# Kernel tuning notes

Hardware: AMD Instinct MI355X
Metric: run time of the kernel (lower is better)

## Reference

```python
import jax, jax.numpy as jnp
import numpy as np

D_MODEL, D_STATE, D_CONV, EXPAND = 1024, 16, 4, 2
D_INNER = EXPAND * D_MODEL
B, L = 2, 2048


def setup_inputs() -> dict:
    key = jax.random.key(0)
    ks = jax.random.split(key, 8)
    s = lambda fan: 1.0 / np.sqrt(fan)
    x = jax.random.normal(ks[0], (B, L, D_MODEL), dtype=jnp.float32)
    W_in = jax.random.normal(ks[1], (2 * D_INNER, D_MODEL), dtype=jnp.float32) * s(D_MODEL)
    conv_w = jax.random.normal(ks[2], (D_INNER, 1, D_CONV), dtype=jnp.float32) * s(D_CONV)
    conv_b = jax.random.normal(ks[3], (D_INNER,), dtype=jnp.float32) * 0.01
    A_log = jnp.log(jnp.abs(jax.random.normal(ks[4], (D_INNER, D_STATE), dtype=jnp.float32)) + 1e-4)
    Dp = jnp.ones((D_INNER,), dtype=jnp.float32)
    W_dt = jax.random.normal(ks[5], (D_INNER, D_INNER), dtype=jnp.float32) * s(D_INNER)
    b_dt = jax.random.normal(ks[6], (D_INNER,), dtype=jnp.float32) * 0.01
    W_out = jax.random.normal(ks[7], (D_MODEL, D_INNER), dtype=jnp.float32) * s(D_INNER)
    return {"x": x, "W_in": W_in, "conv_w": conv_w, "conv_b": conv_b,
            "A_log": A_log, "Dp": Dp, "W_dt": W_dt, "b_dt": b_dt, "W_out": W_out}


def _mamba_fwd(x, W_in, conv_w, conv_b, A_log, Dp, W_dt, b_dt, W_out):
    Bsz, Ln, _ = x.shape
    xz = x @ W_in.T                                  # [B, L, 2*d_inner]
    x_proj, z = jnp.split(xz, 2, axis=-1)            # each [B, L, d_inner]
    # depthwise causal conv1d: left-pad d_conv-1 (matches torch pad + [:L] slice)
    xc = jnp.transpose(x_proj, (0, 2, 1))            # [B, C, L]
    xc = jax.lax.conv_general_dilated(
        xc, conv_w, window_strides=(1,), padding=[(D_CONV - 1, 0)],
        dimension_numbers=("NCH", "OIH", "NCH"), feature_group_count=D_INNER)
    xc = xc + conv_b[None, :, None]
    x_act = jax.nn.silu(jnp.transpose(xc, (0, 2, 1)))  # [B, L, d_inner]
    dt = jax.nn.softplus(x_act @ W_dt.T + b_dt)        # [B, L, d_inner]
    A = -jnp.exp(A_log)                                # [d_inner, d_state]

    def step(h, inp):
        xt, dt_t = inp                                 # [B, d_inner] each
        dA = jnp.exp(dt_t[:, :, None] * A[None])       # [B, d_inner, d_state]
        dB = (dt_t * xt)[:, :, None]                   # broadcast over states
        h = dA * h + dB
        y_t = h.sum(axis=-1) + Dp * xt                 # [B, d_inner]
        return h, y_t

    h0 = jnp.zeros((Bsz, D_INNER, D_STATE), dtype=x.dtype)
    xs = (jnp.transpose(x_act, (1, 0, 2)), jnp.transpose(dt, (1, 0, 2)))  # [L, B, d_inner]
    _, ys = jax.lax.scan(step, h0, xs)
    y_ssm = jnp.transpose(ys, (1, 0, 2))               # [B, L, d_inner]
    y_gated = y_ssm * jax.nn.silu(z)
    return y_gated @ W_out.T                           # [B, L, d_model]


def reference(x, W_in, conv_w, conv_b, A_log, Dp, W_dt, b_dt, W_out):
    return _mamba_fwd(x, W_in, conv_w, conv_b, A_log, Dp, W_dt, b_dt, W_out)
```

## Files before the change

kernel.cpp:

```cpp
#include <hip/hip_runtime.h>

#define DMODEL 1024
#define DSTATE 16
#define DCONV  4
#define DINNER 2048
#define BSZ    2
#define LSEQ   2048
#define MTOT   (BSZ * LSEQ)
#define NCH    64
#define LC     (LSEQ / NCH)
#define LOG2E  1.44269504088896f

typedef unsigned short u16;
typedef __attribute__((ext_vector_type(8))) short short8;
typedef __attribute__((ext_vector_type(8))) unsigned short u16x8;
typedef __attribute__((ext_vector_type(4))) float f32x4;

__device__ __forceinline__ float silu_f(float v) {
  return v * __builtin_amdgcn_rcpf(1.f + __builtin_amdgcn_exp2f(-v * LOG2E));
}

__device__ __forceinline__ u16 f2bf(float f) {
  unsigned int u = __float_as_uint(f);
  u += 0x7FFF + ((u >> 16) & 1);
  return (u16)(u >> 16);
}
__device__ __forceinline__ float bf2f(u16 b) { return __uint_as_float(((unsigned int)b) << 16); }

__device__ __forceinline__ void gload_lds16(const u16* g, u16* l) {
  __builtin_amdgcn_global_load_lds((const __attribute__((address_space(1))) unsigned int*)g,
                                   (__attribute__((address_space(3))) unsigned int*)l, 16, 0, 0);
}

__global__ __launch_bounds__(256)
void cast4(const float4* __restrict__ s0, ushort4* __restrict__ d0, int n0,
           const float4* __restrict__ s1, ushort4* __restrict__ d1, int n1,
           const float4* __restrict__ s2, ushort4* __restrict__ d2, int n2,
           const float4* __restrict__ s3, ushort4* __restrict__ d3, int n3) {
  int i = blockIdx.x * 256 + threadIdx.x;
  const float4* s; ushort4* d;
  if (i < n0)                { s = s0; d = d0; }
  else if ((i -= n0) < n1)   { s = s1; d = d1; }
  else if ((i -= n1) < n2)   { s = s2; d = d2; }
  else if ((i -= n2) < n3)   { s = s3; d = d3; }
  else return;
  float4 v = s[i];
  ushort4 o = { f2bf(v.x), f2bf(v.y), f2bf(v.z), f2bf(v.w) };
  d[i] = o;
}

template<int BN, int MODE, int OBF>
__global__ __launch_bounds__(512, 2)
void gemm8p(const u16* __restrict__ A, const u16* __restrict__ Bm,
            const float* __restrict__ bias, void* __restrict__ Cv,
            int M, int N, int K) {
  constexpr int BT  = BN / 32;
  constexpr int TJP = 2;
  constexpr int NPH = BT / TJP;
  constexpr int NBH = BN / 128;
  extern __shared__ __align__(16) u16 smem[];
  u16* As = smem;
  u16* Bs = smem + 2 * 256 * 64;

  const int tid  = threadIdx.x;
  const int lane = tid & 63;
  const int w    = tid >> 6;
  const int quad = lane >> 4;
  const int l16  = lane & 15;
  const int wm   = (w >> 1) * 64;
  const int wn   = (w & 1) * (BN / 2);

  const int nbn = N / BN, nbm = M >> 8;
  const int pid = blockIdx.x;
  const int npg = 4 * nbn;
  const int fm  = (pid / npg) * 4;
  const int gsz = (nbm - fm < 4) ? (nbm - fm) : 4;
  const int bm  = (fm + (pid % gsz)) << 8;
  const int bn  = ((pid % npg) / gsz) * BN;

  const int rseg = lane >> 3;
  const int cd8  = (((lane & 7) ^ rseg) << 3);
  const int browB = (BN == 64) ? (8 * w) : (16 * w);
  const u16* gA = A  + (size_t)(bm + 16 * w + rseg) * K + cd8;
  const u16* gB = Bm + (size_t)(bn + browB + rseg) * K + cd8;
  u16* lA = &As[(2 * w) << 9];
  u16* lB = (BN == 64) ? &Bs[w << 9] : &Bs[(2 * w) << 9];
  const int Kmask = K - 1;

  auto stA = [&](int slot, int h, int kt) {
    const size_t go = (size_t)h * 128 * K + ((kt << 6) & Kmask);
    gload_lds16(gA + go,         lA + slot * 16384 + h * 8192);
    gload_lds16(gA + go + 8 * K, lA + slot * 16384 + h * 8192 + 512);
  };
  auto stB = [&](int slot, int h, int kt) {
    const size_t go = (size_t)h * 128 * K + ((kt << 6) & Kmask);
    if constexpr (BN == 64) {
      gload_lds16(gB + go, lB + slot * (BN * 64));
    } else {
      gload_lds16(gB + go,         lB + slot * (BN * 64) + h * 8192);
      gload_lds16(gB + go + 8 * K, lB + slot * (BN * 64) + h * 8192 + 512);
    }
  };

  int aoff[4][2], boff[BT][2];
#pragma unroll
  for (int t = 0; t < 4; ++t) {
    const int ra = wm + 16 * t + l16;
#pragma unroll
    for (int ks = 0; ks < 2; ++ks)
      aoff[t][ks] = ra * 64 + (((quad + 4 * ks) ^ (ra & 7)) << 3);
  }
#pragma unroll
  for (int tj = 0; tj < BT; ++tj) {
    const int rb = wn + 16 * tj + l16;
#pragma unroll
    for (int ks = 0; ks < 2; ++ks)
      boff[tj][ks] = rb * 64 + (((quad + 4 * ks) ^ (rb & 7)) << 3);
  }

  f32x4 acc[4][BT] = {};
  short8 af[4][2];

#define RD_AF(slot)                                                          \
  { _Pragma("unroll") for (int t = 0; t < 4; ++t)                            \
      _Pragma("unroll") for (int ks = 0; ks < 2; ++ks)                       \
        af[t][ks] = *(const short8*)&As[(slot) * 16384 + aoff[t][ks]]; }

#define VM4 asm volatile("s_waitcnt vmcnt(4)" ::: "memory")
#define NOWAIT ((void)0)

#define PHASE(slot, j, STG, WAIT)                                            \
  {                                                                          \
    if ((j) == 0) RD_AF(slot);                                               \
    short8 bfp[TJP][2];                                                      \
    _Pragma("unroll") for (int jj = 0; jj < TJP; ++jj)                       \
      _Pragma("unroll") for (int ks = 0; ks < 2; ++ks)                       \
        bfp[jj][ks] = *(const short8*)&Bs[(slot) * (BN * 64) +               \
                                          boff[(j) * TJP + jj][ks]];         \
    STG;                                                                     \
    __builtin_amdgcn_s_setprio(1);                                           \
    _Pragma("unroll") for (int ks = 0; ks < 2; ++ks)                         \
      _Pragma("unroll") for (int jj = 0; jj < TJP; ++jj)                     \
        _Pragma("unroll") for (int t = 0; t < 4; ++t)                        \
          acc[t][(j) * TJP + jj] = __builtin_amdgcn_mfma_f32_16x16x32_bf16(  \
              af[t][ks], bfp[jj][ks], acc[t][(j) * TJP + jj], 0, 0, 0);      \
    __builtin_amdgcn_s_setprio(0);                                           \
    asm volatile("s_waitcnt lgkmcnt(0)" ::: "memory");                       \
    WAIT;                                                                    \
    __builtin_amdgcn_s_barrier();                                            \
  }

  stA(0, 0, 0); stA(0, 1, 0);
  stB(0, 0, 0); if (NBH == 2) stB(0, 1, 0);
  stA(1, 0, 1); stA(1, 1, 1);
  VM4;
  __builtin_amdgcn_s_barrier();

  const int niter = K >> 7;
  for (int i = 0; i < niter; ++i) {
    const int tb1 = 2 * i + 1, t2 = 2 * i + 2, t3 = 2 * i + 3;
    if constexpr (NPH == 4) {
      PHASE(0, 0, { stB(1, 0, tb1); },               NOWAIT);
      PHASE(0, 1, { stB(1, 1, tb1); stA(0, 0, t2); }, NOWAIT);
      PHASE(0, 2, { stA(0, 1, t2); },                NOWAIT);
      PHASE(0, 3, {},                                VM4);
      PHASE(1, 0, { stB(0, 0, t2); },                NOWAIT);
      PHASE(1, 1, { stB(0, 1, t2); stA(1, 0, t3); }, NOWAIT);
      PHASE(1, 2, { stA(1, 1, t3); },                NOWAIT);
      PHASE(1, 3, {},                                VM4);
    } else if constexpr (NPH == 2) {
      PHASE(0, 0, { stB(1, 0, tb1); },                NOWAIT);
      PHASE(0, 1, { stA(0, 0, t2); stA(0, 1, t2); },  VM4);
      PHASE(1, 0, { stB(0, 0, t2); },                 NOWAIT);
      PHASE(1, 1, { stA(1, 0, t3); stA(1, 1, t3); },  VM4);
    } else {
      PHASE(0, 0, { stB(1, 0, tb1); stA(0, 0, t2); stA(0, 1, t2); }, VM4);
      PHASE(1, 0, { stB(0, 0, t2);  stA(1, 0, t3); stA(1, 1, t3); }, VM4);
    }
  }
#undef PHASE
#undef RD_AF
#undef VM4
#undef NOWAIT

  asm volatile("s_waitcnt vmcnt(0)" ::: "memory");
  __builtin_amdgcn_s_barrier();

  constexpr int WTN = BN / 2;
  if constexpr (OBF) {
    constexpr int CPR = WTN / 8;
    u16* patch = smem + (size_t)w * (64 * WTN);
#pragma unroll
    for (int t = 0; t < 4; ++t) {
#pragma unroll
      for (int tj = 0; tj < BT; ++tj) {
        const int colb = 16 * tj + l16;
        const float bv = (MODE == 1) ? bias[bn + wn + colb] : 0.f;
#pragma unroll
        for (int i2 = 0; i2 < 4; ++i2) {
          const int row = 16 * t + quad * 4 + i2;
          float v = acc[t][tj][i2] + bv;
          if (MODE == 1) v = (v > 20.f) ? v : __logf(1.f + __expf(v));
          patch[row * WTN + ((((colb >> 3) ^ (row & (CPR - 1))) << 3) | (colb & 7))] = f2bf(v);
        }
      }
    }
    asm volatile("s_waitcnt lgkmcnt(0)" ::: "memory");
#pragma unroll
    for (int it = 0; it < CPR; ++it) {
      const int flat = it * 64 + lane;
      const int row  = flat / CPR;
      const int cc   = flat % CPR;
      const u16x8 vv = *(const u16x8*)&patch[row * WTN + ((cc ^ (row & (CPR - 1))) << 3)];
      *(u16x8*)((u16*)Cv + (size_t)(bm + wm + row) * N + bn + wn + cc * 8) = vv;
    }
  } else {
    constexpr int CPR = WTN / 4;
    float* patch = (float*)smem + (size_t)w * (64 * WTN);
#pragma unroll
    for (int t = 0; t < 4; ++t) {
#pragma unroll
      for (int tj = 0; tj < BT; ++tj) {
        const int colb = 16 * tj + l16;
#pragma unroll
        for (int i2 = 0; i2 < 4; ++i2) {
          const int row = 16 * t + quad * 4 + i2;
          patch[row * WTN + ((((colb >> 2) ^ (row & (CPR - 1))) << 2) | (colb & 3))] =
              acc[t][tj][i2];
        }
      }
    }
    asm volatile("s_waitcnt lgkmcnt(0)" ::: "memory");
#pragma unroll
    for (int it = 0; it < CPR; ++it) {
      const int flat = it * 64 + lane;
      const int row  = flat / CPR;
      const int cc   = flat % CPR;
      const float4 vv = *(const float4*)&patch[row * WTN + ((cc ^ (row & (CPR - 1))) << 2)];
      *(float4*)((float*)Cv + (size_t)(bm + wm + row) * N + bn + wn + cc * 4) = vv;
    }
  }
}

__global__ __launch_bounds__(256)
void conv_silu(const u16* __restrict__ xz, const float* __restrict__ conv_w,
               const float* __restrict__ conv_b, u16* __restrict__ xact) {
  const int i = blockIdx.x * 256 + threadIdx.x;
  const int ko = i & 255;
  const int t  = (i >> 8) & (LSEQ - 1);
  const int b  = i >> 19;
  const int c  = ko << 3;
  float a[8];
  float4 w[8];
#pragma unroll
  for (int j = 0; j < 8; ++j) {
    a[j] = conv_b[c + j];
    w[j] = *(const float4*)(conv_w + (c + j) * DCONV);
  }
#pragma unroll
  for (int k = 0; k < DCONV; ++k) {
    const int tt = t + k - (DCONV - 1);
    if (tt >= 0) {
      const u16x8 v = *(const u16x8*)(xz + ((size_t)(b * LSEQ + tt) << 12) + c);
#pragma unroll
      for (int j = 0; j < 8; ++j)
        a[j] = fmaf(bf2f(v[j]), ((const float*)&w[j])[k], a[j]);
    }
  }
  u16x8 o;
#pragma unroll
  for (int j = 0; j < 8; ++j) o[j] = f2bf(silu_f(a[j]));
  *(u16x8*)(xact + ((size_t)(b * LSEQ + t) << 11) + c) = o;
}


__global__ __launch_bounds__(256, 2)
void scan_pass1(const u16* __restrict__ dtb, const u16* __restrict__ xact,
                const float* __restrict__ A_log,
                u16* __restrict__ hbuf, float* __restrict__ sumdt) {
  const int gid = blockIdx.x * 256 + threadIdx.x;
  const int c  = gid & (DINNER - 1);
  const int ch = (gid >> 11) & (NCH - 1);
  const int b  = gid >> 17;
  float a2[16];
#pragma unroll
  for (int s = 0; s < 16; ++s)
    a2[s] = -__expf(A_log[c * DSTATE + s]) * LOG2E;
  const size_t base = ((size_t)(b * LSEQ + ch * LC) << 11) + c;
  float h[16] = {};
  float sd = 0.f;
  for (int j = 0; j < LC; j += 2) {
    const float dt0 = bf2f(dtb [base + ((size_t)j << 11)]);
    const float xv0 = bf2f(xact[base + ((size_t)j << 11)]);
    const float dt1 = bf2f(dtb [base + ((size_t)(j + 1) << 11)]);
    const float xv1 = bf2f(xact[base + ((size_t)(j + 1) << 11)]);
    const float dx0 = dt0 * xv0, dx1 = dt1 * xv1;
    sd += dt0 + dt1;
#pragma unroll
    for (int s = 0; s < 16; ++s)
      h[s] = fmaf(__builtin_amdgcn_exp2f(dt0 * a2[s]), h[s], dx0);
#pragma unroll
    for (int s = 0; s < 16; ++s)
      h[s] = fmaf(__builtin_amdgcn_exp2f(dt1 * a2[s]), h[s], dx1);
  }
  u16x8* ho = (u16x8*)&hbuf[(((size_t)(b * NCH + ch) * DINNER) + c) << 4];
  u16x8 lo, hi;
#pragma unroll
  for (int s = 0; s < 8; ++s) { lo[s] = f2bf(h[s]); hi[s] = f2bf(h[8 + s]); }
  ho[0] = lo; ho[1] = hi;
  sumdt[(size_t)(b * NCH + ch) * DINNER + c] = sd;
}

__global__ __launch_bounds__(256)
void scan_combine(u16* __restrict__ hbuf, const float* __restrict__ sumdt,
                  const float* __restrict__ A_log) {
  const int gid = blockIdx.x * 256 + threadIdx.x;
  const int s = gid & 15;
  const int c = (gid >> 4) & (DINNER - 1);
  const int b = gid >> 15;
  const float a2 = -__expf(A_log[c * DSTATE + s]) * LOG2E;
  float h = 0.f;
  for (int k = 0; k < NCH; ++k) {
    const size_t o = (((size_t)(b * NCH + k) * DINNER) + c) * 16 + s;
    const float he = bf2f(hbuf[o]);
    const float sd = sumdt[(size_t)(b * NCH + k) * DINNER + c];
    hbuf[o] = f2bf(h);
    h = fmaf(__builtin_amdgcn_exp2f(sd * a2), h, he);
  }
}

__global__ __launch_bounds__(256, 2)
void scan_pass3(const u16* __restrict__ dtb, const u16* __restrict__ xact,
                const u16* __restrict__ xz, const float* __restrict__ A_log,
                const float* __restrict__ Dp, const u16* __restrict__ hbuf,
                u16* __restrict__ yg) {
  const int gid = blockIdx.x * 256 + threadIdx.x;
  const int c  = gid & (DINNER - 1);
  const int ch = (gid >> 11) & (NCH - 1);
  const int b  = gid >> 17;
  float a2[16];
#pragma unroll
  for (int s = 0; s < 16; ++s)
    a2[s] = -__expf(A_log[c * DSTATE + s]) * LOG2E;
  const float dp = Dp[c];
  float h[16];
  const u16x8* hi = (const u16x8*)&hbuf[(((size_t)(b * NCH + ch) * DINNER) + c) << 4];
  const u16x8 vlo = hi[0], vhi = hi[1];
#pragma unroll
  for (int s = 0; s < 8; ++s) { h[s] = bf2f(vlo[s]); h[8 + s] = bf2f(vhi[s]); }
  const size_t base  = ((size_t)(b * LSEQ + ch * LC) << 11) + c;
  const size_t zbase = ((size_t)(b * LSEQ + ch * LC) << 12) + DINNER + c;
  for (int j = 0; j < LC; j += 2) {
    const float dt0 = bf2f(dtb [base + ((size_t)j << 11)]);
    const float xv0 = bf2f(xact[base + ((size_t)j << 11)]);
    const float zv0 = bf2f(xz[zbase + ((size_t)j << 12)]);
    const float dt1 = bf2f(dtb [base + ((size_t)(j + 1) << 11)]);
    const float xv1 = bf2f(xact[base + ((size_t)(j + 1) << 11)]);
    const float zv1 = bf2f(xz[zbase + ((size_t)(j + 1) << 12)]);
    const float dx0 = dt0 * xv0, dx1 = dt1 * xv1;
    float y0 = 0.f, y1 = 0.f;
#pragma unroll
    for (int s = 0; s < 16; ++s) {
      h[s] = fmaf(__builtin_amdgcn_exp2f(dt0 * a2[s]), h[s], dx0);
      y0 += h[s];
    }
#pragma unroll
    for (int s = 0; s < 16; ++s) {
      h[s] = fmaf(__builtin_amdgcn_exp2f(dt1 * a2[s]), h[s], dx1);
      y1 += h[s];
    }
    y0 = fmaf(dp, xv0, y0);
    y1 = fmaf(dp, xv1, y1);
    yg[base + ((size_t)j << 11)]       = f2bf(y0 * silu_f(zv0));
    yg[base + ((size_t)(j + 1) << 11)] = f2bf(y1 * silu_f(zv1));
  }
}

extern "C" void kernel_launch(void* const* d_in, const int* in_sizes, int n_in,
                              void* d_out, int out_size, void* d_ws, size_t ws_size,
                              hipStream_t stream) {
  const float* x      = (const float*)d_in[0];
  const float* W_in   = (const float*)d_in[1];
  const float* conv_w = (const float*)d_in[2];
  const float* conv_b = (const float*)d_in[3];
  const float* A_log  = (const float*)d_in[4];
  const float* Dp     = (const float*)d_in[5];
  const float* W_dt   = (const float*)d_in[6];
  const float* b_dt   = (const float*)d_in[7];
  const float* W_out  = (const float*)d_in[8];
  float* out = (float*)d_out;

  u16* xz   = (u16*)d_ws;
  u16* dtb  = xz   + (size_t)MTOT * 2 * DINNER;
  u16* xbf  = dtb  + (size_t)MTOT * DINNER;
  u16* wibf = xbf  + (size_t)MTOT * DMODEL;
  u16* wdbf = wibf + (size_t)2 * DINNER * DMODEL;
  u16* wobf = wdbf + (size_t)DINNER * DINNER;
  u16* xact = wobf + (size_t)DMODEL * DINNER;
  u16* yg   = xact + (size_t)MTOT * DINNER;
  u16* hbuf = yg   + (size_t)MTOT * DINNER;
  float* sumdt = (float*)(hbuf + (size_t)BSZ * NCH * DINNER * 16);

  const dim3 blk(256);

  static bool s_attr = false;
  if (!s_attr) {
    hipFuncSetAttribute(reinterpret_cast<const void*>(&gemm8p<256, 0, 1>),
                        hipFuncAttributeMaxDynamicSharedMemorySize, 131072);
    hipFuncSetAttribute(reinterpret_cast<const void*>(&gemm8p<128, 1, 1>),
                        hipFuncAttributeMaxDynamicSharedMemorySize, 98304);
    hipFuncSetAttribute(reinterpret_cast<const void*>(&gemm8p<64, 0, 0>),
                        hipFuncAttributeMaxDynamicSharedMemorySize, 81920);
    s_attr = true;
  }

  const int n0 = MTOT * DMODEL / 4, n1 = 2 * DINNER * DMODEL / 4;
  const int n2 = DINNER * DINNER / 4, n3 = DMODEL * DINNER / 4;
  cast4<<<(n0 + n1 + n2 + n3) / 256, blk, 0, stream>>>(
      (const float4*)x, (ushort4*)xbf, n0,
      (const float4*)W_in, (ushort4*)wibf, n1,
      (const float4*)W_dt, (ushort4*)wdbf, n2,
      (const float4*)W_out, (ushort4*)wobf, n3);

  gemm8p<256, 0, 1><<<(MTOT / 256) * (2 * DINNER / 256), dim3(512), 131072, stream>>>(
      xbf, wibf, nullptr, xz, MTOT, 2 * DINNER, DMODEL);
  conv_silu<<<(MTOT * 256) / 256, blk, 0, stream>>>(xz, conv_w, conv_b, xact);
  gemm8p<128, 1, 1><<<(MTOT / 256) * (DINNER / 128), dim3(512), 98304, stream>>>(
      xact, wdbf, b_dt, dtb, MTOT, DINNER, DINNER);
  scan_pass1<<<BSZ * NCH * DINNER / 256, blk, 0, stream>>>(dtb, xact, A_log, hbuf, sumdt);
  scan_combine<<<BSZ * DINNER * 16 / 256, blk, 0, stream>>>(hbuf, sumdt, A_log);
  scan_pass3<<<BSZ * NCH * DINNER / 256, blk, 0, stream>>>(dtb, xact, xz, A_log, Dp, hbuf, yg);
  gemm8p<64, 0, 0><<<(MTOT / 256) * (DMODEL / 64), dim3(512), 81920, stream>>>(
      yg, wobf, nullptr, out, MTOT, DMODEL, DINNER);
}
```

Baseline: 293.6 us.

## Use a new 128x128-tile double-buffered GEMM kernel for the dt projection

Adds gemm128, a 256-thread bf16 MFMA GEMM with 128x128 tiles, swizzled LDS, grouped block ordering, and split B loading interleaved with prefetch. It replaces the 512-thread 256x128 gemm8p for the x_act @ W_dt GEMM with fused bias and softplus. The smaller tiles give more blocks (512 vs 256) for better CU fill on this 4096x2048x2048 GEMM, at the cost of less data reuse per tile and scalar bf16 stores in the epilogue.

```diff
diff --git a/kernel.cpp b/kernel.cpp
--- a/kernel.cpp
+++ b/kernel.cpp
@@ -47,6 +47,136 @@
   float4 v = s[i];
   ushort4 o = { f2bf(v.x), f2bf(v.y), f2bf(v.z), f2bf(v.w) };
   d[i] = o;
+}
+
+template<int MODE, int OBF>
+__global__ __launch_bounds__(256)
+void gemm128(const u16* __restrict__ A, const u16* __restrict__ Bm,
+             const float* __restrict__ bias, void* __restrict__ Cv,
+             int M, int N, int K) {
+  __shared__ u16 As[2 * 128 * 64];
+  __shared__ u16 Bs[2 * 128 * 64];
+
+  const int tid  = threadIdx.x;
+  const int lane = tid & 63;
+  const int w    = tid >> 6;
+  const int quad = lane >> 4;
+  const int l16  = lane & 15;
+  const int wm   = (w & 1) * 64;
+  const int wn   = (w >> 1) * 64;
+
+  const int nbn = N >> 7, nbm = M >> 7;
+  const int pid = blockIdx.x;
+  const int npg = 8 * nbn;
+  const int fm  = (pid / npg) * 8;
+  const int gsz = (nbm - fm < 8) ? (nbm - fm) : 8;
+  const int bm  = (fm + (pid % gsz)) << 7;
+  const int bn  = ((pid % npg) / gsz) << 7;
+
+  const int rseg = lane >> 3;
+  const int cd8  = (((lane & 7) ^ rseg) << 3);
+  const u16* gA = A  + (size_t)(bm + 32 * w + rseg) * K + cd8;
+  const u16* gB = Bm + (size_t)(bn + 32 * w + rseg) * K + cd8;
+  u16* lAw = &As[w * 2048];
+  u16* lBw = &Bs[w * 2048];
+  const int Kmask = K - 1;
+
+  auto stA = [&](int slot, int kt) {
+    const int ko = (kt << 6) & Kmask;
+#pragma unroll
+    for (int q = 0; q < 4; ++q)
+      gload_lds16(gA + (size_t)q * 8 * K + ko, lAw + slot * 8192 + q * 512);
+  };
+  auto stB = [&](int slot, int kt) {
+    const int ko = (kt << 6) & Kmask;
+#pragma unroll
+    for (int q = 0; q < 4; ++q)
+      gload_lds16(gB + (size_t)q * 8 * K + ko, lBw + slot * 8192 + q * 512);
+  };
+
+  int aoff[4][2], boff[4][2];
+#pragma unroll
+  for (int t = 0; t < 4; ++t) {
+    const int ra = wm + 16 * t + l16;
+    const int rb = wn + 16 * t + l16;
+#pragma unroll
+    for (int ks = 0; ks < 2; ++ks) {
+      aoff[t][ks] = ra * 64 + (((quad + 4 * ks) ^ (ra & 7)) << 3);
+      boff[t][ks] = rb * 64 + (((quad + 4 * ks) ^ (rb & 7)) << 3);
+    }
+  }
+
+  f32x4 acc[4][4] = {};
+  short8 af[4][2], bf0[2][2], bf1[2][2];
+
+  stA(0, 0); stB(0, 0); stA(1, 1);
+  asm volatile("s_waitcnt vmcnt(4)" ::: "memory");
+  __builtin_amdgcn_s_barrier();
+
+  const int nt = K >> 6;
+  for (int t = 0; t < nt; ++t) {
+    const int s = t & 1;
+#pragma unroll
+    for (int ti = 0; ti < 4; ++ti)
+#pragma unroll
+      for (int ks = 0; ks < 2; ++ks)
+        af[ti][ks] = *(const short8*)&As[s * 8192 + aoff[ti][ks]];
+#pragma unroll
+    for (int tj = 0; tj < 2; ++tj)
+#pragma unroll
+      for (int ks = 0; ks < 2; ++ks)
+        bf0[tj][ks] = *(const short8*)&Bs[s * 8192 + boff[tj][ks]];
+    stB(s ^ 1, t + 1);
+    __builtin_amdgcn_s_setprio(1);
+#pragma unroll
+    for (int ks = 0; ks < 2; ++ks)
+#pragma unroll
+      for (int tj = 0; tj < 2; ++tj)
+#pragma unroll
+        for (int ti = 0; ti < 4; ++ti)
+          acc[ti][tj] = __builtin_amdgcn_mfma_f32_16x16x32_bf16(
+              af[ti][ks], bf0[tj][ks], acc[ti][tj], 0, 0, 0);
+    __builtin_amdgcn_s_setprio(0);
+    asm volatile("s_waitcnt lgkmcnt(0)" ::: "memory");
+    __builtin_amdgcn_s_barrier();
+#pragma unroll
+    for (int tj = 0; tj < 2; ++tj)
+#pragma unroll
+      for (int ks = 0; ks < 2; ++ks)
+        bf1[tj][ks] = *(const short8*)&Bs[s * 8192 + boff[2 + tj][ks]];
+    stA(s, t + 2);
+    __builtin_amdgcn_s_setprio(1);
+#pragma unroll
+    for (int ks = 0; ks < 2; ++ks)
+#pragma unroll
+      for (int tj = 0; tj < 2; ++tj)
+#pragma unroll
+        for (int ti = 0; ti < 4; ++ti)
+          acc[ti][2 + tj] = __builtin_amdgcn_mfma_f32_16x16x32_bf16(
+              af[ti][ks], bf1[tj][ks], acc[ti][2 + tj], 0, 0, 0);
+    __builtin_amdgcn_s_setprio(0);
+    asm volatile("s_waitcnt lgkmcnt(0)" ::: "memory");
+    asm volatile("s_waitcnt vmcnt(4)" ::: "memory");
+    __builtin_amdgcn_s_barrier();
+  }
+  asm volatile("s_waitcnt vmcnt(0)" ::: "memory");
+
+#pragma unroll
+  for (int t = 0; t < 4; ++t) {
+    const int row0 = bm + wm + 16 * t + quad * 4;
+#pragma unroll
+    for (int tj = 0; tj < 4; ++tj) {
+      const int col = bn + wn + 16 * tj + l16;
+      const float bv = (MODE == 1) ? bias[col] : 0.f;
+#pragma unroll
+      for (int i2 = 0; i2 < 4; ++i2) {
+        float v = acc[t][tj][i2] + bv;
+        if (MODE == 1) v = (v > 20.f) ? v : __logf(1.f + __expf(v));
+        if (OBF) ((u16*)Cv)[(size_t)(row0 + i2) * N + col] = f2bf(v);
+        else     ((float*)Cv)[(size_t)(row0 + i2) * N + col] = v;
+      }
+    }
+  }
 }
 
 template<int BN, int MODE, int OBF>
@@ -407,8 +537,6 @@
   if (!s_attr) {
     hipFuncSetAttribute(reinterpret_cast<const void*>(&gemm8p<256, 0, 1>),
                         hipFuncAttributeMaxDynamicSharedMemorySize, 131072);
-    hipFuncSetAttribute(reinterpret_cast<const void*>(&gemm8p<128, 1, 1>),
-                        hipFuncAttributeMaxDynamicSharedMemorySize, 98304);
     hipFuncSetAttribute(reinterpret_cast<const void*>(&gemm8p<64, 0, 0>),
                         hipFuncAttributeMaxDynamicSharedMemorySize, 81920);
     s_attr = true;
@@ -425,7 +553,7 @@
   gemm8p<256, 0, 1><<<(MTOT / 256) * (2 * DINNER / 256), dim3(512), 131072, stream>>>(
       xbf, wibf, nullptr, xz, MTOT, 2 * DINNER, DMODEL);
   conv_silu<<<(MTOT * 256) / 256, blk, 0, stream>>>(xz, conv_w, conv_b, xact);
-  gemm8p<128, 1, 1><<<(MTOT / 256) * (DINNER / 128), dim3(512), 98304, stream>>>(
+  gemm128<1, 1><<<(MTOT / 128) * (DINNER / 128), blk, 0, stream>>>(
       xact, wdbf, b_dt, dtb, MTOT, DINNER, DINNER);
   scan_pass1<<<BSZ * NCH * DINNER / 256, blk, 0, stream>>>(dtb, xact, A_log, hbuf, sumdt);
   scan_combine<<<BSZ * DINNER * 16 / 256, blk, 0, stream>>>(hbuf, sumdt, A_log);
```

New measurement: 303.4 us. 3.4% more time.
